# Kernel tuning notes

Hardware: AMD Instinct MI355X
Metric: run time of the kernel (lower is better)

## Reference

```python
import jax, jax.numpy as jnp
import numpy as np

IN_C, OUT_C, K, PAD = 64, 64, 3, 1
B, H, W = 8, 256, 256


def setup_inputs() -> dict:
    key = jax.random.key(0)
    k1, k2, k3, k4, k5 = jax.random.split(key, 5)
    x = jax.random.normal(k1, (B, IN_C, H, W), jnp.float32)
    # per-output-channel rank-1 CPD factors
    w1 = jax.random.normal(k2, (OUT_C, IN_C), jnp.float32) * 0.1   # 1x1 conv weights
    wh = jax.random.normal(k3, (OUT_C, K), jnp.float32) * 0.3      # 1xK horizontal kernels
    wv = jax.random.normal(k4, (OUT_C, K), jnp.float32) * 0.3      # Kx1 vertical kernels
    bias = jax.random.normal(k5, (OUT_C,), jnp.float32) * 0.01
    return {"x": x, "w1": w1, "wh": wh, "wv": wv, "bias": bias}


def _depthwise(y, w, kh, kw, ph, pw):
    # y: [B, C, H, W]; w: [C, kh*kw] -> depthwise conv with groups=C
    C = y.shape[1]
    kern = w.reshape(C, 1, kh, kw)
    return jax.lax.conv_general_dilated(
        y, kern, window_strides=(1, 1), padding=((ph, ph), (pw, pw)),
        dimension_numbers=("NCHW", "OIHW", "NCHW"), feature_group_count=C)


def reference(x, w1, wh, wv, bias):
    # Fused form of the per-branch loop: all branches share structure
    # 1x1 projection over in_channels -> one channel per branch
    y = jnp.einsum("bchw,oc->bohw", x, w1)          # [B, O, H, W]
    y = _depthwise(y, wh, 1, K, 0, PAD)              # 1xK horizontal conv
    y = _depthwise(y, wv, K, 1, PAD, 0)              # Kx1 vertical conv (bias last)
    return y + bias[None, :, None, None]
```

## Files before the change

### kernel.cpp

```cpp
#include <hip/hip_runtime.h>

#define NUM_B 8
#define NUM_C 64
#define NUM_O 64
#define DIM_H 256
#define DIM_W 256
#define SEG   8
#define TPB   512
#define XSS   72

typedef __attribute__((ext_vector_type(8))) short bf16x8;
typedef __attribute__((ext_vector_type(4))) float f32x4;

__device__ __forceinline__ unsigned bf16r(float f) {
    unsigned u = __float_as_uint(f);
    return (u + 0x7fffu + ((u >> 16) & 1u)) >> 16;
}
__device__ __forceinline__ unsigned cvt_pk_bf16(float lo, float hi) {
    unsigned r;
    asm("v_cvt_pk_bf16_f32 %0, %1, %2" : "=v"(r) : "v"(lo), "v"(hi));
    return r;
}

__global__ __launch_bounds__(TPB, 2)
void cpd_mfma(const float* __restrict__ x, const float* __restrict__ w1,
              const float* __restrict__ wh, const float* __restrict__ wv,
              const float* __restrict__ bias, float* __restrict__ out)
{
    __shared__ unsigned short xs[DIM_W + 2][XSS];

    const int tid  = threadIdx.x;
    const int lane = tid & 63;
    const int wave = tid >> 6;
    const int l15  = lane & 15;
    const int lhi  = lane >> 4;
    const int bx   = blockIdx.x;
    const int b    = bx >> 5;
    const int h0   = (bx & 31) * SEG;

    const int ot  = wave & 3;
    const int wh2 = wave >> 2;

    bf16x8 afrag[3][2];
    {
        const int o = ot * 16 + l15;
        const float a0 = wh[o*3+0], a1 = wh[o*3+1], a2 = wh[o*3+2];
        #pragma unroll
        for (int kb = 0; kb < 2; ++kb) {
            const float* wr = w1 + o * NUM_C + kb * 32 + lhi * 8;
            const float4 wa = *(const float4*)wr;
            const float4 wb = *(const float4*)(wr + 4);
            const float w8[8] = {wa.x,wa.y,wa.z,wa.w,wb.x,wb.y,wb.z,wb.w};
            #pragma unroll
            for (int i = 0; i < 8; ++i) {
                afrag[0][kb][i] = (short)bf16r(a0 * w8[i]);
                afrag[1][kb][i] = (short)bf16r(a1 * w8[i]);
                afrag[2][kb][i] = (short)bf16r(a2 * w8[i]);
            }
        }
    }
    float v0c[4], v1c[4], v2c[4], bc[4];
    #pragma unroll
    for (int r = 0; r < 4; ++r) {
        const int o = ot * 16 + lhi * 4 + r;
        v0c[r] = wv[o*3+0]; v1c[r] = wv[o*3+1]; v2c[r] = wv[o*3+2];
        bc[r]  = bias[o];
    }

    if (tid < XSS) { xs[0][tid] = 0; xs[DIM_W + 1][tid] = 0; }

    const int sw = tid & 255;
    const int ch = tid >> 8;
    const float* xb = x + (size_t)b * NUM_C * DIM_H * DIM_W + sw;

    float xr[32];
    if (h0 > 0) {
        #pragma unroll
        for (int p = 0; p < 8; ++p) {
            const int c0 = p * 8 + ch * 4;
            #pragma unroll
            for (int j = 0; j < 4; ++j)
                xr[p*4+j] = xb[(size_t)(c0+j) * (DIM_H*DIM_W) + (size_t)(h0-1) * DIM_W];
        }
    }

    f32x4 zP[8], zPP[8];
    #pragma unroll
    for (int t = 0; t < 8; ++t) {
        zP[t]  = (f32x4){0.f,0.f,0.f,0.f};
        zPP[t] = (f32x4){0.f,0.f,0.f,0.f};
    }

    for (int hh = -1; hh <= SEG; ++hh) {
        const int h = h0 + hh;
        const bool hv = (h >= 0) && (h < DIM_H);

        __builtin_amdgcn_s_barrier();
        __builtin_amdgcn_sched_barrier(0);

        if (hv) {
            #pragma unroll
            for (int p = 0; p < 8; ++p) {
                const unsigned lo = cvt_pk_bf16(xr[p*4+0], xr[p*4+1]);
                const unsigned hi = cvt_pk_bf16(xr[p*4+2], xr[p*4+3]);
                *(uint2*)&xs[sw + 1][p * 8 + ch * 4] = make_uint2(lo, hi);
            }
        }
        if (hh < SEG && h + 1 < DIM_H) {
            #pragma unroll
            for (int p = 0; p < 8; ++p) {
                const int c0 = p * 8 + ch * 4;
                #pragma unroll
                for (int j = 0; j < 4; ++j)
                    xr[p*4+j] = xb[(size_t)(c0+j) * (DIM_H*DIM_W) + (size_t)(h+1) * DIM_W];
            }
        }

        asm volatile("s_waitcnt lgkmcnt(0)" ::: "memory");
        __builtin_amdgcn_s_barrier();
        __builtin_amdgcn_sched_barrier(0);

        f32x4 acc[8];
        #pragma unroll
        for (int t = 0; t < 8; ++t) acc[t] = (f32x4){0.f,0.f,0.f,0.f};

        if (hv) {
            const int cb = lhi * 8;
            #pragma unroll
            for (int t = 0; t < 8; ++t) {
                const unsigned short* rp0 = &xs[wh2 * 128 + t * 16 + l15][cb];
                #pragma unroll
                for (int s = 0; s < 3; ++s) {
                    const unsigned short* rp = rp0 + s * XSS;
                    const bf16x8 b0 = *(const bf16x8*)rp;
                    const bf16x8 b1 = *(const bf16x8*)(rp + 32);
                    acc[t] = __builtin_amdgcn_mfma_f32_16x16x32_bf16(afrag[s][0], b0, acc[t], 0, 0, 0);
                    acc[t] = __builtin_amdgcn_mfma_f32_16x16x32_bf16(afrag[s][1], b1, acc[t], 0, 0, 0);
                }
            }
        }

        if (hh >= 1) {
            float* ob = out + (size_t)b * NUM_O * DIM_H * DIM_W + (size_t)(h - 1) * DIM_W;
            #pragma unroll
            for (int t = 0; t < 8; ++t) {
                const int w = wh2 * 128 + t * 16 + l15;
                #pragma unroll
                for (int r = 0; r < 4; ++r) {
                    const int o = ot * 16 + lhi * 4 + r;
                    ob[(size_t)o * (DIM_H * DIM_W) + w] =
                        bc[r] + v0c[r]*zPP[t][r] + v1c[r]*zP[t][r] + v2c[r]*acc[t][r];
                }
            }
        }

        #pragma unroll
        for (int t = 0; t < 8; ++t) { zPP[t] = zP[t]; zP[t] = acc[t]; }
    }
}

extern "C" void kernel_launch(void* const* d_in, const int* in_sizes, int n_in,
                              void* d_out, int out_size, void* d_ws, size_t ws_size,
                              hipStream_t stream) {
    const float* x    = (const float*)d_in[0];
    const float* w1   = (const float*)d_in[1];
    const float* wh   = (const float*)d_in[2];
    const float* wv   = (const float*)d_in[3];
    const float* bias = (const float*)d_in[4];
    float* outp = (float*)d_out;
    cpd_mfma<<<dim3(NUM_B * (DIM_H / SEG)), dim3(TPB), 0, stream>>>(x, w1, wh, wv, bias, outp);
}
```

Before: 59.56 us.

## Double block size, ping-pong row prefetch two ahead, stage vertical weights in LDS

Raises the block from 512 to 1024 threads (16 waves), so each wave computes 4 width tiles instead of 8 and each thread loads 16 input channels instead of 32. Row loads alternate between two register buffers and are issued two rows ahead, so global loads have more time in flight. Vertical weights and bias move from per-thread registers into shared memory and are read per output row. The aim is more latency hiding and lower per-thread register pressure, at the cost of a larger block that may limit occupancy and extra LDS reads in the epilogue.

Measured after the change: 173.1 us. 2.91x slower.

```diff
diff --git a/kernel.cpp b/kernel.cpp
--- a/kernel.cpp
+++ b/kernel.cpp
@@ -6,7 +6,7 @@
 #define DIM_H 256
 #define DIM_W 256
 #define SEG   8
-#define TPB   512
+#define TPB   1024
 #define XSS   72
 
 typedef __attribute__((ext_vector_type(8))) short bf16x8;
@@ -22,12 +22,13 @@
     return r;
 }
 
-__global__ __launch_bounds__(TPB, 2)
+__global__ __launch_bounds__(TPB, 4)
 void cpd_mfma(const float* __restrict__ x, const float* __restrict__ w1,
               const float* __restrict__ wh, const float* __restrict__ wv,
               const float* __restrict__ bias, float* __restrict__ out)
 {
     __shared__ unsigned short xs[DIM_W + 2][XSS];
+    __shared__ float wvb[NUM_O][4];
 
     const int tid  = threadIdx.x;
     const int lane = tid & 63;
@@ -38,8 +39,8 @@
     const int b    = bx >> 5;
     const int h0   = (bx & 31) * SEG;
 
-    const int ot  = wave & 3;
-    const int wh2 = wave >> 2;
+    const int ot = wave & 3;
+    const int wd = wave >> 2;
 
     bf16x8 afrag[3][2];
     {
@@ -59,104 +60,106 @@
             }
         }
     }
-    float v0c[4], v1c[4], v2c[4], bc[4];
-    #pragma unroll
-    for (int r = 0; r < 4; ++r) {
-        const int o = ot * 16 + lhi * 4 + r;
-        v0c[r] = wv[o*3+0]; v1c[r] = wv[o*3+1]; v2c[r] = wv[o*3+2];
-        bc[r]  = bias[o];
-    }
 
     if (tid < XSS) { xs[0][tid] = 0; xs[DIM_W + 1][tid] = 0; }
+    if (tid < NUM_O) {
+        wvb[tid][0] = wv[tid*3+0];
+        wvb[tid][1] = wv[tid*3+1];
+        wvb[tid][2] = wv[tid*3+2];
+        wvb[tid][3] = bias[tid];
+    }
 
     const int sw = tid & 255;
     const int ch = tid >> 8;
     const float* xb = x + (size_t)b * NUM_C * DIM_H * DIM_W + sw;
 
-    float xr[32];
+    float xrA[16], xrB[16];
     if (h0 > 0) {
         #pragma unroll
-        for (int p = 0; p < 8; ++p) {
-            const int c0 = p * 8 + ch * 4;
+        for (int q = 0; q < 4; ++q)
             #pragma unroll
             for (int j = 0; j < 4; ++j)
-                xr[p*4+j] = xb[(size_t)(c0+j) * (DIM_H*DIM_W) + (size_t)(h0-1) * DIM_W];
-        }
+                xrA[q*4+j] = xb[(size_t)(ch*16+q*4+j)*(DIM_H*DIM_W) + (size_t)(h0-1)*DIM_W];
     }
+    #pragma unroll
+    for (int q = 0; q < 4; ++q)
+        #pragma unroll
+        for (int j = 0; j < 4; ++j)
+            xrB[q*4+j] = xb[(size_t)(ch*16+q*4+j)*(DIM_H*DIM_W) + (size_t)h0*DIM_W];
 
-    f32x4 zP[8], zPP[8];
+    f32x4 zP[4], zPP[4];
     #pragma unroll
-    for (int t = 0; t < 8; ++t) {
-        zP[t]  = (f32x4){0.f,0.f,0.f,0.f};
-        zPP[t] = (f32x4){0.f,0.f,0.f,0.f};
+    for (int t = 0; t < 4; ++t) { zP[t] = (f32x4){0,0,0,0}; zPP[t] = (f32x4){0,0,0,0}; }
+
+    __syncthreads();
+
+#define STEP(HH, XR)                                                                      \
+    do {                                                                                  \
+        const int  h  = h0 + (HH);                                                        \
+        const bool hv = (h >= 0) && (h < DIM_H);                                          \
+        __builtin_amdgcn_s_barrier();                                        \
+        __builtin_amdgcn_sched_barrier(0);                                                \
+        if (hv) {                                                                         \
+            _Pragma("unroll")                                                             \
+            for (int q = 0; q < 4; ++q) {                                                 \
+                const unsigned lo = cvt_pk_bf16(XR[q*4+0], XR[q*4+1]);                    \
+                const unsigned hi = cvt_pk_bf16(XR[q*4+2], XR[q*4+3]);                    \
+                *(uint2*)&xs[sw + 1][ch * 16 + q * 4] = make_uint2(lo, hi);               \
+            }                                                                             \
+        }                                                                                 \
+        if ((HH) <= SEG - 2 && h + 2 < DIM_H) {           \
+            _Pragma("unroll")                                                             \
+            for (int q = 0; q < 4; ++q)                                                   \
+                _Pragma("unroll")                                                         \
+                for (int j = 0; j < 4; ++j)                                               \
+                    XR[q*4+j] = xb[(size_t)(ch*16+q*4+j)*(DIM_H*DIM_W)                    \
+                                   + (size_t)(h+2)*DIM_W];                                \
+        }                                                                                 \
+        asm volatile("s_waitcnt lgkmcnt(0)" ::: "memory");                                \
+        __builtin_amdgcn_s_barrier();                     \
+        __builtin_amdgcn_sched_barrier(0);                                                \
+        f32x4 acc[4];                                                                     \
+        _Pragma("unroll")                                                                 \
+        for (int t = 0; t < 4; ++t) acc[t] = (f32x4){0.f,0.f,0.f,0.f};                    \
+        if (hv) {                                                                         \
+            const int cb = lhi * 8;                                                       \
+            _Pragma("unroll")                                                             \
+            for (int t = 0; t < 4; ++t) {                                                 \
+                const unsigned short* rp0 = &xs[wd*64 + t*16 + l15][cb];                  \
+                _Pragma("unroll")                                                         \
+                for (int s = 0; s < 3; ++s) {                                             \
+                    const unsigned short* rp = rp0 + s * XSS;                             \
+                    const bf16x8 b0 = *(const bf16x8*)rp;                                 \
+                    const bf16x8 b1 = *(const bf16x8*)(rp + 32);                          \
+                    acc[t] = __builtin_amdgcn_mfma_f32_16x16x32_bf16(afrag[s][0], b0, acc[t], 0,0,0); \
+                    acc[t] = __builtin_amdgcn_mfma_f32_16x16x32_bf16(afrag[s][1], b1, acc[t], 0,0,0); \
+                }                                                                         \
+            }                                                                             \
+        }                                                                                 \
+        if ((HH) >= 1) {                                    \
+            const int g = h - 1;                                                          \
+            _Pragma("unroll")                                                             \
+            for (int r = 0; r < 4; ++r) {                                                 \
+                const int o = ot * 16 + lhi * 4 + r;                                      \
+                const float4 cf = *(const float4*)wvb[o];                                 \
+                float* ob = out + ((size_t)(b * NUM_O + o) * DIM_H + g) * DIM_W           \
+                                + wd * 64 + l15;                                          \
+                _Pragma("unroll")                                                         \
+                for (int t = 0; t < 4; ++t)                                               \
+                    ob[t * 16] = cf.w + cf.x * zPP[t][r] + cf.y * zP[t][r]                \
+                                      + cf.z * acc[t][r];                                 \
+            }                                                                             \
+        }                                                                                 \
+        _Pragma("unroll")                                                                 \
+        for (int t = 0; t < 4; ++t) { zPP[t] = zP[t]; zP[t] = acc[t]; }                   \
+    } while (0)
+
+    #pragma unroll
+    for (int p = 0; p < (SEG + 2) / 2; ++p) {
+        STEP(2 * p - 1, xrA);
+        STEP(2 * p,     xrB);
     }
-
-    for (int hh = -1; hh <= SEG; ++hh) {
-        const int h = h0 + hh;
-        const bool hv = (h >= 0) && (h < DIM_H);
-
-        __builtin_amdgcn_s_barrier();
-        __builtin_amdgcn_sched_barrier(0);
-
-        if (hv) {
-            #pragma unroll
-            for (int p = 0; p < 8; ++p) {
-                const unsigned lo = cvt_pk_bf16(xr[p*4+0], xr[p*4+1]);
-                const unsigned hi = cvt_pk_bf16(xr[p*4+2], xr[p*4+3]);
-                *(uint2*)&xs[sw + 1][p * 8 + ch * 4] = make_uint2(lo, hi);
-            }
-        }
-        if (hh < SEG && h + 1 < DIM_H) {
-            #pragma unroll
-            for (int p = 0; p < 8; ++p) {
-                const int c0 = p * 8 + ch * 4;
-                #pragma unroll
-                for (int j = 0; j < 4; ++j)
-                    xr[p*4+j] = xb[(size_t)(c0+j) * (DIM_H*DIM_W) + (size_t)(h+1) * DIM_W];
-            }
-        }
-
-        asm volatile("s_waitcnt lgkmcnt(0)" ::: "memory");
-        __builtin_amdgcn_s_barrier();
-        __builtin_amdgcn_sched_barrier(0);
-
-        f32x4 acc[8];
-        #pragma unroll
-        for (int t = 0; t < 8; ++t) acc[t] = (f32x4){0.f,0.f,0.f,0.f};
-
-        if (hv) {
-            const int cb = lhi * 8;
-            #pragma unroll
-            for (int t = 0; t < 8; ++t) {
-                const unsigned short* rp0 = &xs[wh2 * 128 + t * 16 + l15][cb];
-                #pragma unroll
-                for (int s = 0; s < 3; ++s) {
-                    const unsigned short* rp = rp0 + s * XSS;
-                    const bf16x8 b0 = *(const bf16x8*)rp;
-                    const bf16x8 b1 = *(const bf16x8*)(rp + 32);
-                    acc[t] = __builtin_amdgcn_mfma_f32_16x16x32_bf16(afrag[s][0], b0, acc[t], 0, 0, 0);
-                    acc[t] = __builtin_amdgcn_mfma_f32_16x16x32_bf16(afrag[s][1], b1, acc[t], 0, 0, 0);
-                }
-            }
-        }
-
-        if (hh >= 1) {
-            float* ob = out + (size_t)b * NUM_O * DIM_H * DIM_W + (size_t)(h - 1) * DIM_W;
-            #pragma unroll
-            for (int t = 0; t < 8; ++t) {
-                const int w = wh2 * 128 + t * 16 + l15;
-                #pragma unroll
-                for (int r = 0; r < 4; ++r) {
-                    const int o = ot * 16 + lhi * 4 + r;
-                    ob[(size_t)o * (DIM_H * DIM_W) + w] =
-                        bc[r] + v0c[r]*zPP[t][r] + v1c[r]*zP[t][r] + v2c[r]*acc[t][r];
-                }
-            }
-        }
-
-        #pragma unroll
-        for (int t = 0; t < 8; ++t) { zPP[t] = zP[t]; zP[t] = acc[t]; }
-    }
+#undef STEP
 }
 
 extern "C" void kernel_launch(void* const* d_in, const int* in_sizes, int n_in,
```
